# Performance work log

Measured on AMD Instinct MI355X. Metric: run time of the kernel, lower is better.

## Reference

```python
import jax, jax.numpy as jnp
import numpy as np

NUM_MARGINALS = 8
NUM_NODES = 128
BOX_LOWER = -4.0
BOX_UPPER = 4.0


def _coefficients(nodal_values):
    # Natural cubic spline coefficients per marginal.
    n = NUM_NODES
    h = (BOX_UPPER - BOX_LOWER) / (n - 1)  # uniform step size
    diag = jnp.ones(n, dtype=nodal_values.dtype).at[1:-1].set(4.0)
    sup = jnp.ones(n - 1, dtype=nodal_values.dtype).at[0].set(0.0)
    sub = jnp.ones(n - 1, dtype=nodal_values.dtype).at[-1].set(0.0)
    A = jnp.diag(diag) + jnp.diag(sup, 1) + jnp.diag(sub, -1)  # (n, n) tridiagonal
    rhs = jnp.zeros((NUM_MARGINALS, n), dtype=nodal_values.dtype)
    rhs = rhs.at[:, 1:-1].set(
        3.0 * (nodal_values[:, :-2] - 2.0 * nodal_values[:, 1:-1] + nodal_values[:, 2:]) / (h * h)
    )
    c = jnp.linalg.solve(A, rhs.T).T                      # (f, n)  2nd-order coeffs
    b = (nodal_values[:, 1:] - nodal_values[:, :-1]) / h - h * (2.0 * c[:, :-1] + c[:, 1:]) / 3.0  # (f, n-1)
    d = (c[:, 1:] - c[:, :-1]) / (3.0 * h)                # (f, n-1)
    return nodal_values, b, c, d


def reference(x, nodal_values):
    n = NUM_NODES
    bs, f, w, h_sp = x.shape
    nodes = jnp.linspace(BOX_LOWER, BOX_UPPER, n, dtype=x.dtype)
    # bucketise: clamp(ceil(scaled * (n-1)) - 1, 0, n-2)
    x_scaled = (x - BOX_LOWER) / (BOX_UPPER - BOX_LOWER)
    idx = jnp.clip(jnp.ceil(x_scaled * (n - 1)).astype(jnp.int32) - 1, 0, n - 2)  # (bs,f,w,h)
    y = x - nodes[idx]
    a_t, b_t, c_t, d_t = _coefficients(nodal_values)
    idx_f = jnp.transpose(idx, (1, 0, 2, 3)).reshape(f, -1)  # (f, bs*w*h)

    def gather(coeff):
        g = jnp.take_along_axis(coeff, idx_f, axis=1)
        return jnp.transpose(g.reshape(f, bs, w, h_sp), (1, 0, 2, 3))

    a = gather(a_t)
    b = gather(b_t)
    c = gather(c_t)
    d = gather(d_t)
    # cubic Horner evaluation + global sum
    return jnp.sum(a + y * (b + y * (c + y * d)))


def setup_inputs() -> dict:
    key = jax.random.key(0)
    k1, k2 = jax.random.split(key)
    x = jax.random.normal(k1, (32, 8, 256, 256), dtype=jnp.float32)
    nodal_values = jax.random.normal(k2, (NUM_MARGINALS, NUM_NODES), dtype=jnp.float32)
    return {"x": x, "nodal_values": nodal_values}
```

## Files before the change

kernel.cpp:

```cpp
#include <hip/hip_runtime.h>

#define NM 8
#define NN 128
#define NI 127

#define GRID 2048
#define PT 8

struct WTab { float v[33 * 128]; };
constexpr WTab make_wt() {
    WTab t{};
    double cp[NI];
    cp[0] = 0.0;
    for (int i = 1; i <= 126; ++i) cp[i] = 1.0 / (4.0 - cp[i - 1]);
    for (int i0 = 1; i0 <= 126; ++i0) {
        double dp[NN] = {};
        double prev = 0.0;
        for (int i = 1; i <= 126; ++i) {
            double rhs = (i == i0) ? 1.0 : 0.0;
            prev = (rhs - prev) * cp[i];
            dp[i] = prev;
        }
        double w[NN] = {};
        double cn = 0.0;
        for (int i = 126; i >= 1; --i) {
            cn = dp[i] - cp[i] * cn;
            w[i] = cn;
        }
        for (int k = 0; k < 33; ++k) {
            int j = i0 - 16 + k;
            if (j >= 1 && j <= 126) t.v[k * 128 + i0] = (float)w[j];
        }
    }
    return t;
}
__constant__ WTab WT = make_wt();

__device__ __forceinline__ float eval1(float xv,
                                       const float2* __restrict__ tAB,
                                       const float2* __restrict__ tCD) {
    float t = xv + 4.0f;
    int idx = (int)ceilf(t * 15.875f) - 1;
    idx = min(max(idx, 0), NI - 1);
    float y = fmaf((float)idx, -(8.0f / 127.0f), t);
    float2 ab = tAB[idx];
    float2 cd = tCD[idx];
    return fmaf(y, fmaf(y, fmaf(y, cd.y, cd.x), ab.y), ab.x);
}

__global__ __launch_bounds__(256)
void spline_fused_kernel(const float4* __restrict__ x,
                         const float* __restrict__ nodal,
                         float* __restrict__ partials, int n4) {
    __shared__ float  rhsPad[NM][160];
    __shared__ float  sc[NM][NN];
    __shared__ float2 tabAB[NM * NI];
    __shared__ float2 tabCD[NM * NI];
    __shared__ float  wsum[4];

    const int tid = threadIdx.x;
    const int gid = blockIdx.x * 256 + tid;
    const int S   = GRID * 256;

    float4 v[PT];
    bool full = (gid + (PT - 1) * S < n4);
    if (full) {
        #pragma unroll
        for (int k = 0; k < PT; ++k) v[k] = x[gid + k * S];
    }

    const float inv_h2 = (127.0f / 8.0f) * (127.0f / 8.0f);
    #pragma unroll
    for (int u = 0; u < 5; ++u) {
        int t = tid + u * 256;
        int f = t / 160, j = t - f * 160;
        int jc = j - 16;
        float val = 0.0f;
        if (jc >= 1 && jc <= 126)
            val = 3.0f * (nodal[f * NN + jc - 1] - 2.0f * nodal[f * NN + jc]
                          + nodal[f * NN + jc + 1]) * inv_h2;
        rhsPad[f][j] = val;
    }
    __syncthreads();

    {
        const int i = tid & 127;
        const int g = tid >> 7;
        float a0 = 0.f, a1 = 0.f, a2 = 0.f, a3 = 0.f;
        for (int k = 0; k < 33; ++k) {
            float w = WT.v[k * 128 + i];
            a0 = fmaf(w, rhsPad[g    ][i + k], a0);
            a1 = fmaf(w, rhsPad[g + 2][i + k], a1);
            a2 = fmaf(w, rhsPad[g + 4][i + k], a2);
            a3 = fmaf(w, rhsPad[g + 6][i + k], a3);
        }
        sc[g    ][i] = a0;
        sc[g + 2][i] = a1;
        sc[g + 4][i] = a2;
        sc[g + 6][i] = a3;
    }
    __syncthreads();

    const float h = 8.0f / 127.0f, inv_h = 127.0f / 8.0f;
    for (int t = tid; t < NM * NI; t += 256) {
        int f = t / NI, i = t - f * NI;
        float ci  = sc[f][i];
        float ci1 = sc[f][i + 1];
        float a = nodal[f * NN + i];
        float b = (nodal[f * NN + i + 1] - a) * inv_h - h * (2.0f * ci + ci1) * (1.0f / 3.0f);
        float d = (ci1 - ci) * inv_h * (1.0f / 3.0f);
        tabAB[t] = make_float2(a, b);
        tabCD[t] = make_float2(ci, d);
    }
    __syncthreads();

    const int f = (gid >> 14) & 7;
    const float2* __restrict__ tAB = tabAB + f * NI;
    const float2* __restrict__ tCD = tabCD + f * NI;

    float acc = 0.0f;
    if (full) {
        #pragma unroll
        for (int k = 0; k < PT; ++k) {
            acc += eval1(v[k].x, tAB, tCD);
            acc += eval1(v[k].y, tAB, tCD);
            acc += eval1(v[k].z, tAB, tCD);
            acc += eval1(v[k].w, tAB, tCD);
        }
    } else {
        for (int k = 0; k < PT; ++k) {
            int i = gid + k * S;
            if (i < n4) {
                float4 vv = x[i];
                acc += eval1(vv.x, tAB, tCD); acc += eval1(vv.y, tAB, tCD);
                acc += eval1(vv.z, tAB, tCD); acc += eval1(vv.w, tAB, tCD);
            }
        }
    }

    #pragma unroll
    for (int off = 32; off > 0; off >>= 1) acc += __shfl_down(acc, off);
    int lane = tid & 63;
    int wid  = tid >> 6;
    if (lane == 0) wsum[wid] = acc;
    __syncthreads();
    if (tid == 0) partials[blockIdx.x] = wsum[0] + wsum[1] + wsum[2] + wsum[3];
}

__global__ __launch_bounds__(256)
void final_reduce_kernel(const float* __restrict__ partials, float* __restrict__ out) {
    __shared__ float wsum[4];
    float a = 0.0f;
    for (int i = threadIdx.x; i < GRID; i += 256) a += partials[i];
    #pragma unroll
    for (int off = 32; off > 0; off >>= 1) a += __shfl_down(a, off);
    int lane = threadIdx.x & 63, wid = threadIdx.x >> 6;
    if (lane == 0) wsum[wid] = a;
    __syncthreads();
    if (threadIdx.x == 0) out[0] = wsum[0] + wsum[1] + wsum[2] + wsum[3];
}

extern "C" void kernel_launch(void* const* d_in, const int* in_sizes, int n_in,
                              void* d_out, int out_size, void* d_ws, size_t ws_size,
                              hipStream_t stream) {
    const float* x     = (const float*)d_in[0];
    const float* nodal = (const float*)d_in[1];
    float* out      = (float*)d_out;
    float* partials = (float*)d_ws;

    int n4 = in_sizes[0] / 4;

    spline_fused_kernel<<<GRID, 256, 0, stream>>>((const float4*)x, nodal, partials, n4);
    final_reduce_kernel<<<1, 256, 0, stream>>>(partials, out);
}
```

Baseline: 102.5 us.

## Build spline table only for the block's marginal, pack coefficients as float4

Each block touches only one marginal, because its f index is uniform across the block and across all strided loads. It now computes the tridiagonal solve and coefficient table for that single marginal instead of all eight, cutting per-block setup work and shared memory roughly eightfold. The a, b, c, d coefficients are packed into one float4 so each evaluation does a single LDS read instead of two float2 reads. The input loads become nontemporal, and the bucket index is clamped in float. The trade-off is that fewer threads are busy during the shrunken setup phase.

New measurement: 106.6 us. 1.04x slower.

```diff
diff --git a/kernel.cpp b/kernel.cpp
--- a/kernel.cpp
+++ b/kernel.cpp
@@ -36,104 +36,86 @@
 }
 __constant__ WTab WT = make_wt();
 
-__device__ __forceinline__ float eval1(float xv,
-                                       const float2* __restrict__ tAB,
-                                       const float2* __restrict__ tCD) {
-    float t = xv + 4.0f;
-    int idx = (int)ceilf(t * 15.875f) - 1;
-    idx = min(max(idx, 0), NI - 1);
-    float y = fmaf((float)idx, -(8.0f / 127.0f), t);
-    float2 ab = tAB[idx];
-    float2 cd = tCD[idx];
-    return fmaf(y, fmaf(y, fmaf(y, cd.y, cd.x), ab.y), ab.x);
+typedef float f4v __attribute__((ext_vector_type(4)));
+
+__device__ __forceinline__ float eval1(float xv, const float4* __restrict__ tab) {
+    float t  = xv + 4.0f;
+    float fi = ceilf(t * 15.875f) - 1.0f;
+    fi = fminf(fmaxf(fi, 0.0f), 126.0f);
+    int idx = (int)fi;
+    float y = fmaf(fi, -(8.0f / 127.0f), t);
+    float4 co = tab[idx];
+    return fmaf(y, fmaf(y, fmaf(y, co.w, co.z), co.y), co.x);
 }
 
 __global__ __launch_bounds__(256)
-void spline_fused_kernel(const float4* __restrict__ x,
+void spline_fused_kernel(const f4v* __restrict__ x,
                          const float* __restrict__ nodal,
                          float* __restrict__ partials, int n4) {
-    __shared__ float  rhsPad[NM][160];
-    __shared__ float  sc[NM][NN];
-    __shared__ float2 tabAB[NM * NI];
-    __shared__ float2 tabCD[NM * NI];
+    __shared__ float  rhsPad[160];
+    __shared__ float  sc[NN];
+    __shared__ float4 tab[NI];
     __shared__ float  wsum[4];
 
     const int tid = threadIdx.x;
     const int gid = blockIdx.x * 256 + tid;
     const int S   = GRID * 256;
+    const int f   = (gid >> 14) & 7;
 
-    float4 v[PT];
+    f4v v[PT];
     bool full = (gid + (PT - 1) * S < n4);
     if (full) {
         #pragma unroll
-        for (int k = 0; k < PT; ++k) v[k] = x[gid + k * S];
+        for (int k = 0; k < PT; ++k)
+            v[k] = __builtin_nontemporal_load(&x[gid + k * S]);
     }
 
     const float inv_h2 = (127.0f / 8.0f) * (127.0f / 8.0f);
-    #pragma unroll
-    for (int u = 0; u < 5; ++u) {
-        int t = tid + u * 256;
-        int f = t / 160, j = t - f * 160;
-        int jc = j - 16;
+    if (tid < 160) {
+        int jc = tid - 16;
         float val = 0.0f;
         if (jc >= 1 && jc <= 126)
             val = 3.0f * (nodal[f * NN + jc - 1] - 2.0f * nodal[f * NN + jc]
                           + nodal[f * NN + jc + 1]) * inv_h2;
-        rhsPad[f][j] = val;
+        rhsPad[tid] = val;
     }
     __syncthreads();
 
-    {
-        const int i = tid & 127;
-        const int g = tid >> 7;
-        float a0 = 0.f, a1 = 0.f, a2 = 0.f, a3 = 0.f;
-        for (int k = 0; k < 33; ++k) {
-            float w = WT.v[k * 128 + i];
-            a0 = fmaf(w, rhsPad[g    ][i + k], a0);
-            a1 = fmaf(w, rhsPad[g + 2][i + k], a1);
-            a2 = fmaf(w, rhsPad[g + 4][i + k], a2);
-            a3 = fmaf(w, rhsPad[g + 6][i + k], a3);
-        }
-        sc[g    ][i] = a0;
-        sc[g + 2][i] = a1;
-        sc[g + 4][i] = a2;
-        sc[g + 6][i] = a3;
+    if (tid < NN) {
+        float a0 = 0.f;
+        for (int k = 0; k < 33; ++k)
+            a0 = fmaf(WT.v[k * 128 + tid], rhsPad[tid + k], a0);
+        sc[tid] = a0;
     }
     __syncthreads();
 
     const float h = 8.0f / 127.0f, inv_h = 127.0f / 8.0f;
-    for (int t = tid; t < NM * NI; t += 256) {
-        int f = t / NI, i = t - f * NI;
-        float ci  = sc[f][i];
-        float ci1 = sc[f][i + 1];
-        float a = nodal[f * NN + i];
-        float b = (nodal[f * NN + i + 1] - a) * inv_h - h * (2.0f * ci + ci1) * (1.0f / 3.0f);
+    if (tid < NI) {
+        float ci  = sc[tid];
+        float ci1 = sc[tid + 1];
+        float a = nodal[f * NN + tid];
+        float b = (nodal[f * NN + tid + 1] - a) * inv_h - h * (2.0f * ci + ci1) * (1.0f / 3.0f);
         float d = (ci1 - ci) * inv_h * (1.0f / 3.0f);
-        tabAB[t] = make_float2(a, b);
-        tabCD[t] = make_float2(ci, d);
+        tab[tid] = make_float4(a, b, ci, d);
     }
     __syncthreads();
-
-    const int f = (gid >> 14) & 7;
-    const float2* __restrict__ tAB = tabAB + f * NI;
-    const float2* __restrict__ tCD = tabCD + f * NI;
 
     float acc = 0.0f;
     if (full) {
         #pragma unroll
         for (int k = 0; k < PT; ++k) {
-            acc += eval1(v[k].x, tAB, tCD);
-            acc += eval1(v[k].y, tAB, tCD);
-            acc += eval1(v[k].z, tAB, tCD);
-            acc += eval1(v[k].w, tAB, tCD);
+            acc += eval1(v[k].x, tab);
+            acc += eval1(v[k].y, tab);
+            acc += eval1(v[k].z, tab);
+            acc += eval1(v[k].w, tab);
         }
     } else {
         for (int k = 0; k < PT; ++k) {
             int i = gid + k * S;
             if (i < n4) {
-                float4 vv = x[i];
-                acc += eval1(vv.x, tAB, tCD); acc += eval1(vv.y, tAB, tCD);
-                acc += eval1(vv.z, tAB, tCD); acc += eval1(vv.w, tAB, tCD);
+                f4v vv = x[i];
+                acc += eval1(vv.x, tab); acc += eval1(vv.y, tab);
+                acc += eval1(vv.z, tab); acc += eval1(vv.w, tab);
             }
         }
     }
@@ -170,6 +152,6 @@
 
     int n4 = in_sizes[0] / 4;
 
-    spline_fused_kernel<<<GRID, 256, 0, stream>>>((const float4*)x, nodal, partials, n4);
+    spline_fused_kernel<<<GRID, 256, 0, stream>>>((const f4v*)x, nodal, partials, n4);
     final_reduce_kernel<<<1, 256, 0, stream>>>(partials, out);
 }
```
